# Performance work log

Hardware: AMD Instinct MI355X
Metric: run time of the kernel (lower is better)

The kernel has to match this reference:

```python
import jax, jax.numpy as jnp
import numpy as np

EMB = 1536   # emb_dim
RANK = 32
N3 = 204     # modules with in_dim=3840 (6 per layer x 34 layers)
N10 = 34     # modules with in_dim=10240 (1 per layer x 34 layers)


def setup_inputs() -> dict:
    key = jax.random.key(0)
    ks = jax.random.split(key, 9)
    s = lambda k, shp: jax.random.normal(k, shp, dtype=jnp.float32)
    return {
        "x": s(ks[0], (EMB,)),
        "Wp3": s(ks[1], (N3, RANK * RANK, EMB)) * 0.02,   # stacked proj.weight for d=3840 group
        "bp3": s(ks[2], (N3, RANK * RANK)) * 0.02,        # stacked proj.bias
        "Wp10": s(ks[3], (N10, RANK * RANK, EMB)) * 0.02,
        "bp10": s(ks[4], (N10, RANK * RANK)) * 0.02,
        "A3": s(ks[5], (N3, RANK, 3840)),                 # stacked lora_a (rank, in_dim)
        "A10": s(ks[6], (N10, RANK, 10240)),
        "B3": s(ks[7], (N3, 3840, RANK)),                 # stacked lora_b (out_dim, rank); out_dim=3840 group
        "B10": s(ks[8], (N10, 10240, RANK)),
    }


def reference(x, Wp3, bp3, Wp10, bp10, A3, A10, B3, B10):
    # Batched version of the per-module torch loop:
    #   P = proj(x).view(rank, rank);  lora_a_out = P @ lora_a;  lora_b_out = lora_b
    # proj is a GEMV per module -> batched as one einsum per in_dim group.
    P3 = (jnp.einsum('nke,e->nk', Wp3, x) + bp3).reshape(N3, RANK, RANK)    # [N3,32,32]
    P10 = (jnp.einsum('nke,e->nk', Wp10, x) + bp10).reshape(N10, RANK, RANK)  # [N10,32,32]
    la3 = jnp.einsum('nij,njd->nid', P3, A3)      # [N3,32,3840]
    la10 = jnp.einsum('nij,njd->nid', P10, A10)   # [N10,32,10240]
    # lora_b weights are returned unchanged (pass-through), as in the torch module.
    return (la3, la10, B3, B10)
```

## Files before the change

kernel.cpp:

```cpp
#include <hip/hip_runtime.h>

#define EMB   1536
#define RANK  32
#define RANK2 1024
#define N3    204
#define N10   34
#define D3    3840
#define D10   10240

#define ROWS3  (N3 * RANK2)
#define ROWS10 (N10 * RANK2)
#define GEMV_BLOCKS ((ROWS3 + ROWS10) / 4)

#define SZ_LA3  ((size_t)N3  * RANK * D3)
#define SZ_LA10 ((size_t)N10 * RANK * D10)

#define CP_F4_PER_BLOCK 4096
#define CP3_BLOCKS  1530
#define CP10_BLOCKS 680

#define PA3_CHUNKS  4
#define PA10_CHUNKS 10
#define PA3_BLOCKS  (N3 * PA3_CHUNKS)
#define PA10_BLOCKS (N10 * PA10_CHUNKS)

__device__ __forceinline__ void copy_block(const float4* __restrict__ src,
                                           float4* __restrict__ dst,
                                           int chunk) {
    const size_t base = (size_t)chunk * CP_F4_PER_BLOCK + threadIdx.x;
#pragma unroll
    for (int it = 0; it < CP_F4_PER_BLOCK / 256; ++it)
        dst[base + it * 256] = src[base + it * 256];
}

__global__ void k1_gemv_copy(const float* __restrict__ W3,
                             const float* __restrict__ b3,
                             const float* __restrict__ W10,
                             const float* __restrict__ b10,
                             const float* __restrict__ x,
                             float* __restrict__ P3,
                             float* __restrict__ P10,
                             const float4* __restrict__ B3,
                             float4* __restrict__ oB3,
                             const float4* __restrict__ B10,
                             float4* __restrict__ oB10) {
    int bid = blockIdx.x;
    if (bid < GEMV_BLOCKS) {
        const int wave = bid * 4 + (threadIdx.x >> 6);
        const int lane = threadIdx.x & 63;

        const float* W;
        const float* b;
        float* P;
        int row;
        if (wave < ROWS3) {
            W = W3; b = b3; P = P3; row = wave;
        } else {
            W = W10; b = b10; P = P10; row = wave - ROWS3;
        }

        const float* w = W + (size_t)row * EMB;
        float acc = 0.f;
#pragma unroll
        for (int it = 0; it < EMB / 256; ++it) {
            const int e = (it * 64 + lane) * 4;
            const float4 wv = *reinterpret_cast<const float4*>(w + e);
            const float4 xv = *reinterpret_cast<const float4*>(x + e);
            acc = fmaf(wv.x, xv.x, acc);
            acc = fmaf(wv.y, xv.y, acc);
            acc = fmaf(wv.z, xv.z, acc);
            acc = fmaf(wv.w, xv.w, acc);
        }
#pragma unroll
        for (int off = 32; off > 0; off >>= 1)
            acc += __shfl_down(acc, off);
        if (lane == 0) P[row] = acc + b[row];
        return;
    }
    bid -= GEMV_BLOCKS;
    if (bid < CP3_BLOCKS) { copy_block(B3, oB3, bid); return; }
    copy_block(B10, oB10, bid - CP3_BLOCKS);
}

__global__ __launch_bounds__(256) void k2_pa(const float* __restrict__ P3,
                                             const float* __restrict__ A3,
                                             float* __restrict__ la3,
                                             const float* __restrict__ P10,
                                             const float* __restrict__ A10,
                                             float* __restrict__ la10) {
    int bid = blockIdx.x;
    const float* P; const float* A; float* la; int D, m, chunk;
    if (bid < PA3_BLOCKS) {
        m = bid >> 2; chunk = bid & 3;
        P = P3; A = A3; la = la3; D = D3;
    } else {
        bid -= PA3_BLOCKS;
        m = bid / PA10_CHUNKS; chunk = bid % PA10_CHUNKS;
        P = P10; A = A10; la = la10; D = D10;
    }

    __shared__ float Ps[RANK2];
    const float4* Pm4 = reinterpret_cast<const float4*>(P + (size_t)m * RANK2);
    reinterpret_cast<float4*>(Ps)[threadIdx.x] = Pm4[threadIdx.x];
    __syncthreads();

    const int d0 = chunk * 1024 + (int)threadIdx.x * 4;
    if (d0 >= D) return;

    const float* a = A + (size_t)m * RANK * D + d0;
    float4 av[RANK];
#pragma unroll
    for (int j = 0; j < RANK; ++j)
        av[j] = *reinterpret_cast<const float4*>(a + (size_t)j * D);

    const float4* Ps4 = reinterpret_cast<const float4*>(Ps);
    float* o = la + (size_t)m * RANK * D + d0;
#pragma unroll
    for (int i = 0; i < RANK; ++i) {
        float4 pr[8];
#pragma unroll
        for (int j8 = 0; j8 < 8; ++j8)
            pr[j8] = Ps4[i * 8 + j8];
        float4 acc = make_float4(0.f, 0.f, 0.f, 0.f);
#pragma unroll
        for (int j8 = 0; j8 < 8; ++j8) {
            const float4 p4 = pr[j8];
            const float4 a0 = av[j8 * 4 + 0];
            const float4 a1 = av[j8 * 4 + 1];
            const float4 a2 = av[j8 * 4 + 2];
            const float4 a3 = av[j8 * 4 + 3];
            acc.x = fmaf(p4.x, a0.x, acc.x); acc.y = fmaf(p4.x, a0.y, acc.y);
            acc.z = fmaf(p4.x, a0.z, acc.z); acc.w = fmaf(p4.x, a0.w, acc.w);
            acc.x = fmaf(p4.y, a1.x, acc.x); acc.y = fmaf(p4.y, a1.y, acc.y);
            acc.z = fmaf(p4.y, a1.z, acc.z); acc.w = fmaf(p4.y, a1.w, acc.w);
            acc.x = fmaf(p4.z, a2.x, acc.x); acc.y = fmaf(p4.z, a2.y, acc.y);
            acc.z = fmaf(p4.z, a2.z, acc.z); acc.w = fmaf(p4.z, a2.w, acc.w);
            acc.x = fmaf(p4.w, a3.x, acc.x); acc.y = fmaf(p4.w, a3.y, acc.y);
            acc.z = fmaf(p4.w, a3.z, acc.z); acc.w = fmaf(p4.w, a3.w, acc.w);
        }
        *reinterpret_cast<float4*>(o + (size_t)i * D) = acc;
    }
}

extern "C" void kernel_launch(void* const* d_in, const int* in_sizes, int n_in,
                              void* d_out, int out_size, void* d_ws, size_t ws_size,
                              hipStream_t stream) {
    const float* x    = (const float*)d_in[0];
    const float* Wp3  = (const float*)d_in[1];
    const float* bp3  = (const float*)d_in[2];
    const float* Wp10 = (const float*)d_in[3];
    const float* bp10 = (const float*)d_in[4];
    const float* A3   = (const float*)d_in[5];
    const float* A10  = (const float*)d_in[6];
    const float* B3   = (const float*)d_in[7];
    const float* B10  = (const float*)d_in[8];

    float* out = (float*)d_out;

    float* P3  = (float*)d_ws;
    float* P10 = P3 + (size_t)N3 * RANK2;

    float* la3  = out;
    float* la10 = out + SZ_LA3;
    float* oB3  = la10 + SZ_LA10;
    float* oB10 = oB3 + SZ_LA3;

    const int k1_blocks = GEMV_BLOCKS + CP3_BLOCKS + CP10_BLOCKS;
    k1_gemv_copy<<<k1_blocks, 256, 0, stream>>>(
        Wp3, bp3, Wp10, bp10, x, P3, P10,
        (const float4*)B3, (float4*)oB3,
        (const float4*)B10, (float4*)oB10);

    k2_pa<<<PA3_BLOCKS + PA10_BLOCKS, 256, 0, stream>>>(
        P3, A3, la3, P10, A10, la10);
}
```

Before: 375.7 us.

## Move B pass-through copy into PA kernel and process 8 GEMV rows per wave

Moves the lora_b pass-through copy out of the GEMV kernel and into the P@A kernel, so the copy traffic overlaps the second kernel's streaming. Each GEMV wave now computes 8 rows, keeps x in registers for the whole wave, and writes its outputs and biases with vector stores. The copy blocks are also made twice as large. The trade-offs are a longer serial GEMV phase with fewer blocks, and copy blocks competing with the PA blocks for bandwidth.

```diff
diff --git a/kernel.cpp b/kernel.cpp
--- a/kernel.cpp
+++ b/kernel.cpp
@@ -8,87 +8,104 @@
 #define D3    3840
 #define D10   10240
 
-#define ROWS3  (N3 * RANK2)
-#define ROWS10 (N10 * RANK2)
-#define GEMV_BLOCKS ((ROWS3 + ROWS10) / 4)
+#define ROWS3    (N3 * RANK2)
+#define ROWS10   (N10 * RANK2)
+#define ROWS_ALL (ROWS3 + ROWS10)
+
+#define RPW 8
+#define GEMV_BLOCKS (ROWS_ALL / (4 * RPW))
 
 #define SZ_LA3  ((size_t)N3  * RANK * D3)
 #define SZ_LA10 ((size_t)N10 * RANK * D10)
 
-#define CP_F4_PER_BLOCK 4096
-#define CP3_BLOCKS  1530
-#define CP10_BLOCKS 680
+#define CP_F4 8192
+#define CP3_BLOCKS  765
+#define CP10_BLOCKS 340
 
 #define PA3_CHUNKS  4
 #define PA10_CHUNKS 10
 #define PA3_BLOCKS  (N3 * PA3_CHUNKS)
 #define PA10_BLOCKS (N10 * PA10_CHUNKS)
+#define PA_BLOCKS   (PA3_BLOCKS + PA10_BLOCKS)
+
+__global__ __launch_bounds__(256) void k1_gemv(
+    const float* __restrict__ W3, const float* __restrict__ b3,
+    const float* __restrict__ W10, const float* __restrict__ b10,
+    const float* __restrict__ x,
+    float* __restrict__ P3, float* __restrict__ P10)
+{
+    const int wave = blockIdx.x * 4 + (threadIdx.x >> 6);
+    const int lane = threadIdx.x & 63;
+    int r0 = wave * RPW;
+
+    const float* W; const float* b; float* P;
+    if (r0 < ROWS3) { W = W3; b = b3; P = P3; }
+    else            { W = W10; b = b10; P = P10; r0 -= ROWS3; }
+
+    float4 xv[6];
+#pragma unroll
+    for (int it = 0; it < 6; ++it)
+        xv[it] = *reinterpret_cast<const float4*>(x + it * 256 + lane * 4);
+
+    const float* w = W + (size_t)r0 * EMB;
+    float acc[RPW];
+#pragma unroll
+    for (int rr = 0; rr < RPW; ++rr) {
+        float a = 0.f;
+#pragma unroll
+        for (int it = 0; it < 6; ++it) {
+            const float4 wv = *reinterpret_cast<const float4*>(
+                w + (size_t)rr * EMB + it * 256 + lane * 4);
+            a = fmaf(wv.x, xv[it].x, a);
+            a = fmaf(wv.y, xv[it].y, a);
+            a = fmaf(wv.z, xv[it].z, a);
+            a = fmaf(wv.w, xv[it].w, a);
+        }
+        acc[rr] = a;
+    }
+#pragma unroll
+    for (int rr = 0; rr < RPW; ++rr) {
+#pragma unroll
+        for (int off = 32; off > 0; off >>= 1)
+            acc[rr] += __shfl_down(acc[rr], off);
+    }
+    if (lane == 0) {
+        const float4 bv0 = *reinterpret_cast<const float4*>(b + r0);
+        const float4 bv1 = *reinterpret_cast<const float4*>(b + r0 + 4);
+        float4 o0 = make_float4(acc[0] + bv0.x, acc[1] + bv0.y,
+                                acc[2] + bv0.z, acc[3] + bv0.w);
+        float4 o1 = make_float4(acc[4] + bv1.x, acc[5] + bv1.y,
+                                acc[6] + bv1.z, acc[7] + bv1.w);
+        *reinterpret_cast<float4*>(P + r0)     = o0;
+        *reinterpret_cast<float4*>(P + r0 + 4) = o1;
+    }
+}
 
 __device__ __forceinline__ void copy_block(const float4* __restrict__ src,
                                            float4* __restrict__ dst,
                                            int chunk) {
-    const size_t base = (size_t)chunk * CP_F4_PER_BLOCK + threadIdx.x;
+    const size_t base = (size_t)chunk * CP_F4 + threadIdx.x;
 #pragma unroll
-    for (int it = 0; it < CP_F4_PER_BLOCK / 256; ++it)
+    for (int it = 0; it < CP_F4 / 256; ++it)
         dst[base + it * 256] = src[base + it * 256];
 }
 
-__global__ void k1_gemv_copy(const float* __restrict__ W3,
-                             const float* __restrict__ b3,
-                             const float* __restrict__ W10,
-                             const float* __restrict__ b10,
-                             const float* __restrict__ x,
-                             float* __restrict__ P3,
-                             float* __restrict__ P10,
-                             const float4* __restrict__ B3,
-                             float4* __restrict__ oB3,
-                             const float4* __restrict__ B10,
-                             float4* __restrict__ oB10) {
+__global__ __launch_bounds__(256) void k2_pa_copy(
+    const float* __restrict__ P3, const float* __restrict__ A3,
+    float* __restrict__ la3,
+    const float* __restrict__ P10, const float* __restrict__ A10,
+    float* __restrict__ la10,
+    const float4* __restrict__ B3,  float4* __restrict__ oB3,
+    const float4* __restrict__ B10, float4* __restrict__ oB10)
+{
     int bid = blockIdx.x;
-    if (bid < GEMV_BLOCKS) {
-        const int wave = bid * 4 + (threadIdx.x >> 6);
-        const int lane = threadIdx.x & 63;
-
-        const float* W;
-        const float* b;
-        float* P;
-        int row;
-        if (wave < ROWS3) {
-            W = W3; b = b3; P = P3; row = wave;
-        } else {
-            W = W10; b = b10; P = P10; row = wave - ROWS3;
-        }
-
-        const float* w = W + (size_t)row * EMB;
-        float acc = 0.f;
-#pragma unroll
-        for (int it = 0; it < EMB / 256; ++it) {
-            const int e = (it * 64 + lane) * 4;
-            const float4 wv = *reinterpret_cast<const float4*>(w + e);
-            const float4 xv = *reinterpret_cast<const float4*>(x + e);
-            acc = fmaf(wv.x, xv.x, acc);
-            acc = fmaf(wv.y, xv.y, acc);
-            acc = fmaf(wv.z, xv.z, acc);
-            acc = fmaf(wv.w, xv.w, acc);
-        }
-#pragma unroll
-        for (int off = 32; off > 0; off >>= 1)
-            acc += __shfl_down(acc, off);
-        if (lane == 0) P[row] = acc + b[row];
+    if (bid >= PA_BLOCKS) {
+        bid -= PA_BLOCKS;
+        if (bid < CP3_BLOCKS) { copy_block(B3, oB3, bid); return; }
+        copy_block(B10, oB10, bid - CP3_BLOCKS);
         return;
     }
-    bid -= GEMV_BLOCKS;
-    if (bid < CP3_BLOCKS) { copy_block(B3, oB3, bid); return; }
-    copy_block(B10, oB10, bid - CP3_BLOCKS);
-}
 
-__global__ __launch_bounds__(256) void k2_pa(const float* __restrict__ P3,
-                                             const float* __restrict__ A3,
-                                             float* __restrict__ la3,
-                                             const float* __restrict__ P10,
-                                             const float* __restrict__ A10,
-                                             float* __restrict__ la10) {
-    int bid = blockIdx.x;
     const float* P; const float* A; float* la; int D, m, chunk;
     if (bid < PA3_BLOCKS) {
         m = bid >> 2; chunk = bid & 3;
@@ -165,12 +182,10 @@
     float* oB3  = la10 + SZ_LA10;
     float* oB10 = oB3 + SZ_LA3;
 
-    const int k1_blocks = GEMV_BLOCKS + CP3_BLOCKS + CP10_BLOCKS;
-    k1_gemv_copy<<<k1_blocks, 256, 0, stream>>>(
-        Wp3, bp3, Wp10, bp10, x, P3, P10,
+    k1_gemv<<<GEMV_BLOCKS, 256, 0, stream>>>(Wp3, bp3, Wp10, bp10, x, P3, P10);
+
+    k2_pa_copy<<<PA_BLOCKS + CP3_BLOCKS + CP10_BLOCKS, 256, 0, stream>>>(
+        P3, A3, la3, P10, A10, la10,
         (const float4*)B3, (float4*)oB3,
         (const float4*)B10, (float4*)oB10);
-
-    k2_pa<<<PA3_BLOCKS + PA10_BLOCKS, 256, 0, stream>>>(
-        P3, A3, la3, P10, A10, la10);
 }
```

Result: no change. 375.2 us (-0.1%).

## Move B copy into PA kernel interleaved, use nontemporal loads/stores

Applied to the files above, without the earlier changes.

The lora_b pass-through copy moves out of the GEMV kernel and into the P@A kernel. Copy blocks are evenly interleaved with compute blocks so that memory traffic and FMA work mix across the grid. All streaming loads and stores (W, A, B and the outputs) now use nontemporal builtins to avoid polluting caches. This rebalances work between the two kernels and may reduce cache thrash, at the cost of a longer second kernel.

```diff
diff --git a/kernel.cpp b/kernel.cpp
--- a/kernel.cpp
+++ b/kernel.cpp
@@ -8,97 +8,79 @@
 #define D3    3840
 #define D10   10240
 
-#define ROWS3  (N3 * RANK2)
-#define ROWS10 (N10 * RANK2)
-#define GEMV_BLOCKS ((ROWS3 + ROWS10) / 4)
+#define ROWS3    (N3 * RANK2)
+#define ROWS10   (N10 * RANK2)
+#define ROWS_ALL (ROWS3 + ROWS10)
+#define GEMV_BLOCKS (ROWS_ALL / 4)
 
 #define SZ_LA3  ((size_t)N3  * RANK * D3)
 #define SZ_LA10 ((size_t)N10 * RANK * D10)
-
-#define CP_F4_PER_BLOCK 4096
-#define CP3_BLOCKS  1530
-#define CP10_BLOCKS 680
 
 #define PA3_CHUNKS  4
 #define PA10_CHUNKS 10
 #define PA3_BLOCKS  (N3 * PA3_CHUNKS)
 #define PA10_BLOCKS (N10 * PA10_CHUNKS)
+#define NP_BLOCKS   (PA3_BLOCKS + PA10_BLOCKS)
 
-__device__ __forceinline__ void copy_block(const float4* __restrict__ src,
-                                           float4* __restrict__ dst,
-                                           int chunk) {
-    const size_t base = (size_t)chunk * CP_F4_PER_BLOCK + threadIdx.x;
-#pragma unroll
-    for (int it = 0; it < CP_F4_PER_BLOCK / 256; ++it)
-        dst[base + it * 256] = src[base + it * 256];
+#define CP_F4 4096
+#define CP3_BLOCKS  1530
+#define CP10_BLOCKS 680
+#define NC_BLOCKS   (CP3_BLOCKS + CP10_BLOCKS)
+#define NT_BLOCKS   (NP_BLOCKS + NC_BLOCKS)
+
+typedef float float4v __attribute__((ext_vector_type(4)));
+
+__device__ __forceinline__ float4v nt_load4(const float* p) {
+    return __builtin_nontemporal_load(reinterpret_cast<const float4v*>(p));
+}
+__device__ __forceinline__ void nt_store4(float* p, float4v v) {
+    __builtin_nontemporal_store(v, reinterpret_cast<float4v*>(p));
 }
 
-__global__ void k1_gemv_copy(const float* __restrict__ W3,
-                             const float* __restrict__ b3,
-                             const float* __restrict__ W10,
-                             const float* __restrict__ b10,
-                             const float* __restrict__ x,
-                             float* __restrict__ P3,
-                             float* __restrict__ P10,
-                             const float4* __restrict__ B3,
-                             float4* __restrict__ oB3,
-                             const float4* __restrict__ B10,
-                             float4* __restrict__ oB10) {
-    int bid = blockIdx.x;
-    if (bid < GEMV_BLOCKS) {
-        const int wave = bid * 4 + (threadIdx.x >> 6);
-        const int lane = threadIdx.x & 63;
+__global__ __launch_bounds__(256) void k1_gemv(
+    const float* __restrict__ W3, const float* __restrict__ b3,
+    const float* __restrict__ W10, const float* __restrict__ b10,
+    const float* __restrict__ x,
+    float* __restrict__ P3, float* __restrict__ P10)
+{
+    const int wave = blockIdx.x * 4 + (threadIdx.x >> 6);
+    const int lane = threadIdx.x & 63;
 
-        const float* W;
-        const float* b;
-        float* P;
-        int row;
-        if (wave < ROWS3) {
-            W = W3; b = b3; P = P3; row = wave;
-        } else {
-            W = W10; b = b10; P = P10; row = wave - ROWS3;
-        }
+    const float* W; const float* b; float* P; int row;
+    if (wave < ROWS3) { W = W3; b = b3; P = P3; row = wave; }
+    else              { W = W10; b = b10; P = P10; row = wave - ROWS3; }
 
-        const float* w = W + (size_t)row * EMB;
-        float acc = 0.f;
+    const float* w = W + (size_t)row * EMB;
+    float acc = 0.f;
 #pragma unroll
-        for (int it = 0; it < EMB / 256; ++it) {
-            const int e = (it * 64 + lane) * 4;
-            const float4 wv = *reinterpret_cast<const float4*>(w + e);
-            const float4 xv = *reinterpret_cast<const float4*>(x + e);
-            acc = fmaf(wv.x, xv.x, acc);
-            acc = fmaf(wv.y, xv.y, acc);
-            acc = fmaf(wv.z, xv.z, acc);
-            acc = fmaf(wv.w, xv.w, acc);
-        }
+    for (int it = 0; it < EMB / 256; ++it) {
+        const int e = (it * 64 + lane) * 4;
+        const float4v wv = nt_load4(w + e);
+        const float4 xv = *reinterpret_cast<const float4*>(x + e);
+        acc = fmaf(wv.x, xv.x, acc);
+        acc = fmaf(wv.y, xv.y, acc);
+        acc = fmaf(wv.z, xv.z, acc);
+        acc = fmaf(wv.w, xv.w, acc);
+    }
 #pragma unroll
-        for (int off = 32; off > 0; off >>= 1)
-            acc += __shfl_down(acc, off);
-        if (lane == 0) P[row] = acc + b[row];
-        return;
-    }
-    bid -= GEMV_BLOCKS;
-    if (bid < CP3_BLOCKS) { copy_block(B3, oB3, bid); return; }
-    copy_block(B10, oB10, bid - CP3_BLOCKS);
+    for (int off = 32; off > 0; off >>= 1)
+        acc += __shfl_down(acc, off);
+    if (lane == 0) P[row] = acc + b[row];
 }
 
-__global__ __launch_bounds__(256) void k2_pa(const float* __restrict__ P3,
-                                             const float* __restrict__ A3,
-                                             float* __restrict__ la3,
-                                             const float* __restrict__ P10,
-                                             const float* __restrict__ A10,
-                                             float* __restrict__ la10) {
-    int bid = blockIdx.x;
-    const float* P; const float* A; float* la; int D, m, chunk;
-    if (bid < PA3_BLOCKS) {
-        m = bid >> 2; chunk = bid & 3;
-        P = P3; A = A3; la = la3; D = D3;
-    } else {
-        bid -= PA3_BLOCKS;
-        m = bid / PA10_CHUNKS; chunk = bid % PA10_CHUNKS;
-        P = P10; A = A10; la = la10; D = D10;
-    }
+__device__ __forceinline__ void copy_block(const float* __restrict__ src,
+                                           float* __restrict__ dst,
+                                           int chunk) {
+    const size_t base = ((size_t)chunk * CP_F4 + threadIdx.x) * 4;
+#pragma unroll
+    for (int it = 0; it < CP_F4 / 256; ++it)
+        nt_store4(dst + base + (size_t)it * 1024, nt_load4(src + base + (size_t)it * 1024));
+}
 
+__device__ __forceinline__ void pa_block(const float* __restrict__ P,
+                                         const float* __restrict__ A,
+                                         float* __restrict__ la,
+                                         int m, int chunk, int D) {
     __shared__ float Ps[RANK2];
     const float4* Pm4 = reinterpret_cast<const float4*>(P + (size_t)m * RANK2);
     reinterpret_cast<float4*>(Ps)[threadIdx.x] = Pm4[threadIdx.x];
@@ -108,10 +90,10 @@
     if (d0 >= D) return;
 
     const float* a = A + (size_t)m * RANK * D + d0;
-    float4 av[RANK];
+    float4v av[RANK];
 #pragma unroll
     for (int j = 0; j < RANK; ++j)
-        av[j] = *reinterpret_cast<const float4*>(a + (size_t)j * D);
+        av[j] = nt_load4(a + (size_t)j * D);
 
     const float4* Ps4 = reinterpret_cast<const float4*>(Ps);
     float* o = la + (size_t)m * RANK * D + d0;
@@ -121,14 +103,14 @@
 #pragma unroll
         for (int j8 = 0; j8 < 8; ++j8)
             pr[j8] = Ps4[i * 8 + j8];
-        float4 acc = make_float4(0.f, 0.f, 0.f, 0.f);
+        float4v acc = (float4v)(0.f);
 #pragma unroll
         for (int j8 = 0; j8 < 8; ++j8) {
             const float4 p4 = pr[j8];
-            const float4 a0 = av[j8 * 4 + 0];
-            const float4 a1 = av[j8 * 4 + 1];
-            const float4 a2 = av[j8 * 4 + 2];
-            const float4 a3 = av[j8 * 4 + 3];
+            const float4v a0 = av[j8 * 4 + 0];
+            const float4v a1 = av[j8 * 4 + 1];
+            const float4v a2 = av[j8 * 4 + 2];
+            const float4v a3 = av[j8 * 4 + 3];
             acc.x = fmaf(p4.x, a0.x, acc.x); acc.y = fmaf(p4.x, a0.y, acc.y);
             acc.z = fmaf(p4.x, a0.z, acc.z); acc.w = fmaf(p4.x, a0.w, acc.w);
             acc.x = fmaf(p4.y, a1.x, acc.x); acc.y = fmaf(p4.y, a1.y, acc.y);
@@ -138,7 +120,33 @@
             acc.x = fmaf(p4.w, a3.x, acc.x); acc.y = fmaf(p4.w, a3.y, acc.y);
             acc.z = fmaf(p4.w, a3.z, acc.z); acc.w = fmaf(p4.w, a3.w, acc.w);
         }
-        *reinterpret_cast<float4*>(o + (size_t)i * D) = acc;
+        nt_store4(o + (size_t)i * D, acc);
+    }
+}
+
+__global__ __launch_bounds__(256) void k2_pa_copy(
+    const float* __restrict__ P3, const float* __restrict__ A3,
+    float* __restrict__ la3,
+    const float* __restrict__ P10, const float* __restrict__ A10,
+    float* __restrict__ la10,
+    const float* __restrict__ B3,  float* __restrict__ oB3,
+    const float* __restrict__ B10, float* __restrict__ oB10)
+{
+    const int k = blockIdx.x;
+    const int b0 = (int)(((long long)k       * NP_BLOCKS) / NT_BLOCKS);
+    const int b1 = (int)(((long long)(k + 1) * NP_BLOCKS) / NT_BLOCKS);
+    if (b1 > b0) {
+        int idx = b0;
+        if (idx < PA3_BLOCKS) {
+            pa_block(P3, A3, la3, idx >> 2, idx & 3, D3);
+        } else {
+            idx -= PA3_BLOCKS;
+            pa_block(P10, A10, la10, idx / PA10_CHUNKS, idx % PA10_CHUNKS, D10);
+        }
+    } else {
+        int idx = k - b0;
+        if (idx < CP3_BLOCKS) copy_block(B3, oB3, idx);
+        else                  copy_block(B10, oB10, idx - CP3_BLOCKS);
     }
 }
 
@@ -165,12 +173,9 @@
     float* oB3  = la10 + SZ_LA10;
     float* oB10 = oB3 + SZ_LA3;
 
-    const int k1_blocks = GEMV_BLOCKS + CP3_BLOCKS + CP10_BLOCKS;
-    k1_gemv_copy<<<k1_blocks, 256, 0, stream>>>(
-        Wp3, bp3, Wp10, bp10, x, P3, P10,
-        (const float4*)B3, (float4*)oB3,
-        (const float4*)B10, (float4*)oB10);
+    k1_gemv<<<GEMV_BLOCKS, 256, 0, stream>>>(Wp3, bp3, Wp10, bp10, x, P3, P10);
 
-    k2_pa<<<PA3_BLOCKS + PA10_BLOCKS, 256, 0, stream>>>(
-        P3, A3, la3, P10, A10, la10);
+    k2_pa_copy<<<NT_BLOCKS, 256, 0, stream>>>(
+        P3, A3, la3, P10, A10, la10,
+        B3, oB3, B10, oB10);
 }
```

New measurement: 327.8 us. -12.8%, faster.
